# Kernel optimization log

Measured on AMD Instinct MI355X. Metric: run time of the kernel, lower is better.

## Reference

```python
import math
import jax, jax.numpy as jnp
import numpy as np

D, NH, NL, NP = 256, 8, 4, 4
C = D // NH
VALUE_SHAPES = np.array([[128, 128], [64, 64], [32, 32], [16, 16]], dtype=np.int32)


def _offset_bias():
    # Faithful to MSDeformAttn._reset_parameters grid init for sampling_offsets.bias
    th = np.arange(NH, dtype=np.float32) * (2.0 * np.pi / NH)
    g = np.stack([np.cos(th), np.sin(th)], -1)                      # [NH,2]
    g = g / np.abs(g).max(-1, keepdims=True)
    g = np.tile(g[:, None, None, :], (1, NL, NP, 1))                # [NH,NL,NP,2]
    g = g * np.arange(1, NP + 1, dtype=np.float32)[None, None, :, None]
    return jnp.asarray(g.reshape(-1), jnp.float32)


def setup_inputs() -> dict:
    key = jax.random.key(0)
    ks = jax.random.split(key, 10)
    bs, Q = 8, 2048
    LV = int((VALUE_SHAPES[:, 0] * VALUE_SHAPES[:, 1]).sum())
    s = 0.02
    return {
        "query": jax.random.normal(ks[0], (bs, Q, D), jnp.float32),
        "refer_bbox": jax.random.uniform(ks[1], (bs, Q, NL, 2), jnp.float32),
        "value": jax.random.normal(ks[2], (bs, LV, D), jnp.float32),
        "value_shapes": VALUE_SHAPES,  # static numpy (shapes must be compile-time constants)
        "W_value": jax.random.normal(ks[3], (D, D), jnp.float32) * s,
        "b_value": jnp.zeros((D,), jnp.float32),
        "W_off": jax.random.normal(ks[4], (D, NH * NL * NP * 2), jnp.float32) * 0.01,
        "b_off": _offset_bias(),
        "W_attn": jax.random.normal(ks[5], (D, NH * NL * NP), jnp.float32) * s,
        "b_attn": jnp.zeros((NH * NL * NP,), jnp.float32),
        "W_out": jax.random.normal(ks[6], (D, D), jnp.float32) * s,
        "b_out": jnp.zeros((D,), jnp.float32),
    }


def _ms_deform_attn(value, shapes, loc, attn):
    # value: [bs,LV,NH,C], loc: [bs,Q,NH,NL,NP,2] in [0,1], attn: [bs,Q,NH,NL,NP]
    bs, LV = value.shape[:2]
    Q = loc.shape[1]
    BH = bs * NH
    v = value.transpose(0, 2, 1, 3).reshape(BH, LV, C)              # [BH,LV,C]
    loc = loc.transpose(0, 2, 1, 3, 4, 5).reshape(BH, Q, NL, NP, 2)
    attn = attn.transpose(0, 2, 1, 3, 4).reshape(BH, Q, NL, NP)
    acc = jnp.zeros((BH, Q, C), value.dtype)
    start = 0
    for lvl in range(NL):
        H, W = int(shapes[lvl, 0]), int(shapes[lvl, 1])
        img = v[:, start:start + H * W]                             # [BH,HW,C]
        start += H * W
        # grid_sample(align_corners=False): pixel coord = loc * size - 0.5
        x = loc[:, :, lvl, :, 0] * W - 0.5                          # [BH,Q,NP]
        y = loc[:, :, lvl, :, 1] * H - 0.5
        x0 = jnp.floor(x); y0 = jnp.floor(y)
        fx = x - x0; fy = y - y0
        x0i = x0.astype(jnp.int32); y0i = y0.astype(jnp.int32)
        samp = jnp.zeros((BH, Q, NP, C), value.dtype)
        for dx, dy in ((0, 0), (1, 0), (0, 1), (1, 1)):
            xi = x0i + dx; yi = y0i + dy
            valid = (xi >= 0) & (xi < W) & (yi >= 0) & (yi < H)     # zero padding
            w = (fx if dx else 1.0 - fx) * (fy if dy else 1.0 - fy)
            w = jnp.where(valid, w, 0.0)
            idx = jnp.clip(yi, 0, H - 1) * W + jnp.clip(xi, 0, W - 1)
            g = jnp.take_along_axis(img, idx.reshape(BH, Q * NP)[..., None], axis=1)
            samp = samp + w[..., None] * g.reshape(BH, Q, NP, C)
        acc = acc + (samp * attn[:, :, lvl, :, None]).sum(2)
    return acc.reshape(bs, NH, Q, C).transpose(0, 2, 1, 3).reshape(bs, Q, D)


def reference(query, refer_bbox, value, value_shapes, W_value, b_value,
              W_off, b_off, W_attn, b_attn, W_out, b_out):
    shapes = np.asarray(value_shapes)  # static
    bs, Q = query.shape[:2]
    LV = value.shape[1]
    v = (value @ W_value + b_value).reshape(bs, LV, NH, C)
    off = (query @ W_off + b_off).reshape(bs, Q, NH, NL, NP, 2)
    attn = jax.nn.softmax((query @ W_attn + b_attn).reshape(bs, Q, NH, NL * NP), -1)
    attn = attn.reshape(bs, Q, NH, NL, NP)
    norm = jnp.asarray(shapes[:, ::-1], query.dtype)                # (W,H) per level
    loc = refer_bbox[:, :, None, :, None, :] + off / norm[None, None, None, :, None, :]
    out = _ms_deform_attn(v, shapes, loc, attn)
    return out @ W_out + b_out
```

## Files before the change

### kernel.cpp

```cpp
#include <hip/hip_runtime.h>
#include <hip/hip_bf16.h>

#define D_MODEL 256
#define NHEAD   8
#define NLVL    4
#define NPTS    4
#define CH      32
#define QTOT    2048
#define BS      8
#define LVTOT   21760
#define KDIM    256

typedef __attribute__((ext_vector_type(8))) short bf16x8;
typedef __attribute__((ext_vector_type(4))) float f32x4;

__device__ inline float bf_lo(unsigned u) { unsigned t = u << 16; float f; __builtin_memcpy(&f, &t, 4); return f; }
__device__ inline float bf_hi(unsigned u) { unsigned t = u & 0xffff0000u; float f; __builtin_memcpy(&f, &t, 4); return f; }
__device__ inline float bfu2f(unsigned short s) { unsigned t = (unsigned)s << 16; float f; __builtin_memcpy(&f, &t, 4); return f; }
__device__ inline unsigned short f2bfu(float f) { __hip_bfloat16 h = __float2bfloat16(f); unsigned short u; __builtin_memcpy(&u, &h, 2); return u; }

__global__ __launch_bounds__(256)
void convert_W(const float* __restrict__ W, __hip_bfloat16* __restrict__ Wt, int sh) {
    int t = blockIdx.x * 256 + threadIdx.x;
    int k = t >> sh, n = t & ((1 << sh) - 1);
    Wt[n * 256 + k] = __float2bfloat16(W[(k << sh) + n]);
}

__global__ __launch_bounds__(256)
void convert_q(const float* __restrict__ q, __hip_bfloat16* __restrict__ qb) {
    int t = blockIdx.x * 256 + threadIdx.x;
    float4 f = ((const float4*)q)[t];
    __hip_bfloat16 h4[4] = {__float2bfloat16(f.x), __float2bfloat16(f.y),
                            __float2bfloat16(f.z), __float2bfloat16(f.w)};
    ((uint2*)qb)[t] = *(const uint2*)h4;
}

#define BK  64
#define LDP 72
#define LDC2 136

__global__ __launch_bounds__(256, 4)
void gemm_value_mfma(const float* __restrict__ A,
                     const __hip_bfloat16* __restrict__ Wt,
                     const float* __restrict__ bias,
                     __hip_bfloat16* __restrict__ v) {
    __shared__ __align__(16) char smem[128 * LDP * 2 * 2];
    __hip_bfloat16* As = (__hip_bfloat16*)smem;
    __hip_bfloat16* Bs = (__hip_bfloat16*)(smem + 128 * LDP * 2);
    __hip_bfloat16* Cs = (__hip_bfloat16*)smem;

    const int tid  = threadIdx.x;
    const int lane = tid & 63;
    const int wave = tid >> 6;
    const int wr   = wave >> 1;
    const int wc   = wave & 1;
    const int cb      = blockIdx.x * 128;
    const int rowBase = blockIdx.y * 128;

    const int m0   = lane & 15;
    const int quad = lane >> 4;

    const int ar = tid >> 4;
    const int ac = tid & 15;
    const int br = tid >> 3;
    const int bc = tid & 7;

    f32x4 acc[4][4] = {};

    for (int kc = 0; kc < KDIM; kc += BK) {
#pragma unroll
        for (int i = 0; i < 8; ++i) {
            const int row = i * 16 + ar;
            float4 f = *(const float4*)(A + (size_t)(rowBase + row) * KDIM + kc + ac * 4);
            __hip_bfloat16 t4[4] = {__float2bfloat16(f.x), __float2bfloat16(f.y),
                                    __float2bfloat16(f.z), __float2bfloat16(f.w)};
            *(uint2*)&As[row * LDP + ac * 4] = *(const uint2*)t4;
        }
#pragma unroll
        for (int i = 0; i < 4; ++i) {
            const int row = i * 32 + br;
            uint4 u = *(const uint4*)(Wt + (size_t)(cb + row) * KDIM + kc + bc * 8);
            *(uint4*)&Bs[row * LDP + bc * 8] = u;
        }
        __syncthreads();

#pragma unroll
        for (int ks = 0; ks < 2; ++ks) {
            bf16x8 af[4], bfv[4];
#pragma unroll
            for (int i = 0; i < 4; ++i)
                af[i] = *(const bf16x8*)&As[(wr * 64 + i * 16 + m0) * LDP + ks * 32 + quad * 8];
#pragma unroll
            for (int j = 0; j < 4; ++j)
                bfv[j] = *(const bf16x8*)&Bs[(wc * 64 + j * 16 + m0) * LDP + ks * 32 + quad * 8];
#pragma unroll
            for (int i = 0; i < 4; ++i)
#pragma unroll
                for (int j = 0; j < 4; ++j)
                    acc[i][j] = __builtin_amdgcn_mfma_f32_16x16x32_bf16(af[i], bfv[j], acc[i][j], 0, 0, 0);
        }
        __syncthreads();
    }

    const int b = rowBase / LVTOT;
    const int pixBase = rowBase - b * LVTOT;
#pragma unroll
    for (int half = 0; half < 2; ++half) {
        if (wr == half) {
#pragma unroll
            for (int j = 0; j < 4; ++j) {
                const int lcol = wc * 64 + j * 16 + m0;
                const float bv = bias[cb + lcol];
#pragma unroll
                for (int i = 0; i < 4; ++i) {
                    const int lrow = i * 16 + quad * 4;
#pragma unroll
                    for (int r = 0; r < 4; ++r)
                        Cs[(lrow + r) * LDC2 + lcol] = __float2bfloat16(acc[i][j][r] + bv);
                }
            }
        }
        __syncthreads();
        char* dst = (char*)v + (size_t)(b * LVTOT + pixBase + half * 64) * 512 + cb * 2;
        const char* src = (const char*)Cs;
#pragma unroll
        for (int itr = 0; itr < 4; ++itr) {
            const int o = itr * 4096 + tid * 16;
            const int row = o >> 8;
            const int c   = o & 255;
            uint4 val = *(const uint4*)(src + row * (LDC2 * 2) + c);
            *(uint4*)(dst + (size_t)row * 512 + c) = val;
        }
        if (half == 0) __syncthreads();
    }
}

struct StorePlain {
    float* o;
    int ncol;
    __device__ void operator()(int row, int col, float val) const {
        o[(size_t)row * ncol + col] = val;
    }
};

template <typename Store>
__global__ __launch_bounds__(256, 2)
void gemm_bf16_mfma(const __hip_bfloat16* __restrict__ A,
                    const __hip_bfloat16* __restrict__ Wt,
                    const float* __restrict__ bias, Store store) {
    __shared__ __align__(16) __hip_bfloat16 As[128 * LDP];
    __shared__ __align__(16) __hip_bfloat16 Bs[128 * LDP];

    const int tid  = threadIdx.x;
    const int lane = tid & 63;
    const int wave = tid >> 6;
    const int rowBase = blockIdx.x * 128;
    const int cb = blockIdx.y * 128;

    const int m0   = lane & 15;
    const int quad = lane >> 4;

    const int br = tid >> 3;
    const int bc = tid & 7;

    f32x4 acc[2][8] = {};

    for (int kc = 0; kc < KDIM; kc += BK) {
#pragma unroll
        for (int i = 0; i < 4; ++i) {
            const int row = i * 32 + br;
            uint4 ua = *(const uint4*)(A  + (size_t)(rowBase + row) * KDIM + kc + bc * 8);
            uint4 ub = *(const uint4*)(Wt + (size_t)(cb + row) * KDIM + kc + bc * 8);
            *(uint4*)&As[row * LDP + bc * 8] = ua;
            *(uint4*)&Bs[row * LDP + bc * 8] = ub;
        }
        __syncthreads();

#pragma unroll
        for (int ks = 0; ks < 2; ++ks) {
            bf16x8 af[2], bfv[8];
#pragma unroll
            for (int i = 0; i < 2; ++i)
                af[i] = *(const bf16x8*)&As[(wave * 32 + i * 16 + m0) * LDP + ks * 32 + quad * 8];
#pragma unroll
            for (int j = 0; j < 8; ++j)
                bfv[j] = *(const bf16x8*)&Bs[(j * 16 + m0) * LDP + ks * 32 + quad * 8];
#pragma unroll
            for (int i = 0; i < 2; ++i)
#pragma unroll
                for (int j = 0; j < 8; ++j)
                    acc[i][j] = __builtin_amdgcn_mfma_f32_16x16x32_bf16(af[i], bfv[j], acc[i][j], 0, 0, 0);
        }
        __syncthreads();
    }

#pragma unroll
    for (int j = 0; j < 8; ++j) {
        const int col = cb + j * 16 + m0;
        const float bv = bias[col];
#pragma unroll
        for (int i = 0; i < 2; ++i) {
            const int row0 = rowBase + wave * 32 + i * 16 + quad * 4;
#pragma unroll
            for (int r = 0; r < 4; ++r)
                store(row0 + r, col, acc[i][j][r] + bv);
        }
    }
}

__global__ __launch_bounds__(256)
void sample_kernel(const float* __restrict__ off_ws,
                   const float* __restrict__ logits_ws,
                   const float* __restrict__ bbox,
                   const __hip_bfloat16* __restrict__ v,
                   __hip_bfloat16* __restrict__ acc_bf) {
    __shared__ __align__(16) float off_s[8 * 256];
    __shared__ __align__(16) float attn_s[8 * 128];
    __shared__ float bbox_s[64];
    __shared__ __align__(16) int idx_s[1024 * 4];
    __shared__ __align__(8) unsigned short w_s[1024 * 4];

    const int tid = threadIdx.x;
    const int b = blockIdx.x & 7;
    const int gq0 = b * QTOT + (blockIdx.x >> 3) * 8;

    const float4* osrc = (const float4*)(off_ws + (size_t)gq0 * 256);
    ((float4*)off_s)[tid] = osrc[tid];
    ((float4*)off_s)[tid + 256] = osrc[tid + 256];
    const float4* lsrc = (const float4*)(logits_ws + (size_t)gq0 * 128);
    ((float4*)attn_s)[tid] = lsrc[tid];
    if (tid < 64) bbox_s[tid] = bbox[(size_t)gq0 * 8 + tid];
    __syncthreads();

    if (tid < 64) {
        int qq = tid >> 3, h = tid & 7;
        float* p = attn_s + qq * 128 + h * 16;
        float m = p[0];
#pragma unroll
        for (int i = 1; i < 16; ++i) m = fmaxf(m, p[i]);
        float e[16], s = 0.f;
#pragma unroll
        for (int i = 0; i < 16; ++i) { e[i] = __expf(p[i] - m); s += e[i]; }
        float inv = 1.f / s;
#pragma unroll
        for (int i = 0; i < 16; ++i) p[i] = e[i] * inv;
    }
    __syncthreads();

#pragma unroll
    for (int r = 0; r < 4; ++r) {
        const int tap = tid + r * 256;
        const int qq = tap >> 7, h = (tap >> 4) & 7, l = (tap >> 2) & 3, p = tap & 3;
        const int Wd = 128 >> l;
        const int st = (l == 0) ? 0 : (l == 1) ? 16384 : (l == 2) ? 20480 : 21504;

        const float bx = bbox_s[qq * 8 + l * 2 + 0];
        const float by = bbox_s[qq * 8 + l * 2 + 1];
        const float ox = off_s[qq * 256 + h * 32 + l * 8 + p * 2 + 0];
        const float oy = off_s[qq * 256 + h * 32 + l * 8 + p * 2 + 1];
        const float att = attn_s[qq * 128 + h * 16 + l * 4 + p];

        const float x = bx * (float)Wd + ox - 0.5f;
        const float y = by * (float)Wd + oy - 0.5f;
        const float x0f = floorf(x), y0f = floorf(y);
        const float fx = x - x0f, fy = y - y0f;
        const int x0 = (int)x0f, y0 = (int)y0f;
        const int x1 = x0 + 1, y1 = y0 + 1;
        const bool vx0 = (unsigned)x0 < (unsigned)Wd;
        const bool vx1 = (unsigned)x1 < (unsigned)Wd;
        const bool vy0 = (unsigned)y0 < (unsigned)Wd;
        const bool vy1 = (unsigned)y1 < (unsigned)Wd;
        const int cx0 = min(max(x0, 0), Wd - 1), cx1 = min(max(x1, 0), Wd - 1);
        const int cy0 = min(max(y0, 0), Wd - 1), cy1 = min(max(y1, 0), Wd - 1);

        int4 idx;
        idx.x = (st + cy0 * Wd + cx0) << 9;
        idx.y = (st + cy0 * Wd + cx1) << 9;
        idx.z = (st + cy1 * Wd + cx0) << 9;
        idx.w = (st + cy1 * Wd + cx1) << 9;
        float w0 = (vx0 && vy0) ? (1.f - fx) * (1.f - fy) * att : 0.f;
        float w1 = (vx1 && vy0) ? fx * (1.f - fy) * att : 0.f;
        float w2 = (vx0 && vy1) ? (1.f - fx) * fy * att : 0.f;
        float w3 = (vx1 && vy1) ? fx * fy * att : 0.f;

        *(int4*)&idx_s[tap * 4] = idx;
        unsigned short w4[4] = {f2bfu(w0), f2bfu(w1), f2bfu(w2), f2bfu(w3)};
        *(uint2*)&w_s[tap * 4] = *(const uint2*)w4;
    }
    __syncthreads();

    const int lane = tid & 63;
    const int wave = tid >> 6;
    const int g = lane >> 4;
    const int c2 = lane & 15;

    const char* vbase = (const char*)v + (size_t)b * LVTOT * 512 + c2 * 4;

    for (int i = 0; i < 16; ++i) {
        const int pair = wave * 16 + i;
        const int qq = pair >> 3, hh = pair & 7;
        const char* slab = vbase + hh * 64;
        const int tbase = qq * 128 + hh * 16;

        float ax0 = 0.f, ay0 = 0.f, ax1 = 0.f, ay1 = 0.f, ax2 = 0.f, ay2 = 0.f, ax3 = 0.f, ay3 = 0.f;
#pragma unroll
        for (int ts = 0; ts < 4; ++ts) {
            const int tap = tbase + ts * 4 + g;
            const int4 idx = *(const int4*)&idx_s[tap * 4];
            const ushort4 ww = *(const ushort4*)&w_s[tap * 4];
            unsigned u0 = *(const unsigned*)(slab + idx.x);
            unsigned u1 = *(const unsigned*)(slab + idx.y);
            unsigned u2 = *(const unsigned*)(slab + idx.z);
            unsigned u3 = *(const unsigned*)(slab + idx.w);
            float w0 = bfu2f(ww.x), w1 = bfu2f(ww.y), w2 = bfu2f(ww.z), w3 = bfu2f(ww.w);
            ax0 += w0 * bf_lo(u0); ay0 += w0 * bf_hi(u0);
            ax1 += w1 * bf_lo(u1); ay1 += w1 * bf_hi(u1);
            ax2 += w2 * bf_lo(u2); ay2 += w2 * bf_hi(u2);
            ax3 += w3 * bf_lo(u3); ay3 += w3 * bf_hi(u3);
        }
        float sx = (ax0 + ax1) + (ax2 + ax3);
        float sy = (ay0 + ay1) + (ay2 + ay3);
        sx += __shfl_xor(sx, 16); sy += __shfl_xor(sy, 16);
        sx += __shfl_xor(sx, 32); sy += __shfl_xor(sy, 32);
        if (g == 0) {
            __hip_bfloat16 h2[2] = {__float2bfloat16(sx), __float2bfloat16(sy)};
            unsigned packed; __builtin_memcpy(&packed, h2, 4);
            *(unsigned*)((char*)acc_bf + ((size_t)(gq0 + qq) * 256 + hh * 32 + c2 * 2) * 2) = packed;
        }
    }
}

extern "C" void kernel_launch(void* const* d_in, const int* in_sizes, int n_in,
                              void* d_out, int out_size, void* d_ws, size_t ws_size,
                              hipStream_t stream) {
    const float* query   = (const float*)d_in[0];
    const float* bbox    = (const float*)d_in[1];
    const float* value   = (const float*)d_in[2];
    const float* W_value = (const float*)d_in[4];
    const float* b_value = (const float*)d_in[5];
    const float* W_off   = (const float*)d_in[6];
    const float* b_off   = (const float*)d_in[7];
    const float* W_attn  = (const float*)d_in[8];
    const float* b_attn  = (const float*)d_in[9];
    const float* W_out   = (const float*)d_in[10];
    const float* b_out   = (const float*)d_in[11];
    float* out = (float*)d_out;

    char* ws = (char*)d_ws;
    __hip_bfloat16* v_ws  = (__hip_bfloat16*)ws;
    float* off_ws         = (float*)(ws + 89128960);
    float* logits_ws      = (float*)(ws + 89128960 + 16777216);
    __hip_bfloat16* acc_bf = (__hip_bfloat16*)(ws + 89128960 + 16777216 + 8388608);
    __hip_bfloat16* q_bf   = (__hip_bfloat16*)(ws + 89128960 + 16777216 + 8388608 + 8388608);

    __hip_bfloat16* Wt_v    = acc_bf;
    __hip_bfloat16* Wt_off  = acc_bf + 65536;
    __hip_bfloat16* Wt_attn = acc_bf + 131072;
    __hip_bfloat16* Wt_out  = q_bf;

    const int NQ = BS * QTOT;
    const int NVROWS = BS * LVTOT;

    convert_q<<<NQ * KDIM / 1024, 256, 0, stream>>>(query, q_bf);
    convert_W<<<256, 256, 0, stream>>>(W_value, Wt_v, 8);
    convert_W<<<256, 256, 0, stream>>>(W_off, Wt_off, 8);
    convert_W<<<128, 256, 0, stream>>>(W_attn, Wt_attn, 7);

    gemm_value_mfma<<<dim3(2, NVROWS / 128), 256, 0, stream>>>(value, Wt_v, b_value, v_ws);

    gemm_bf16_mfma<<<dim3(NQ / 128, 2), 256, 0, stream>>>(
        q_bf, Wt_off, b_off, StorePlain{off_ws, 256});

    gemm_bf16_mfma<<<dim3(NQ / 128, 1), 256, 0, stream>>>(
        q_bf, Wt_attn, b_attn, StorePlain{logits_ws, 128});

    convert_W<<<256, 256, 0, stream>>>(W_out, Wt_out, 8);

    sample_kernel<<<NQ / 8, 256, 0, stream>>>(off_ws, logits_ws, bbox, v_ws, acc_bf);

    gemm_bf16_mfma<<<dim3(NQ / 128, 2), 256, 0, stream>>>(
        acc_bf, Wt_out, b_out, StorePlain{out, 256});
}
```

Baseline: 415.8 us.

## Merge offset/attention GEMMs and retile value and query GEMMs

The value-projection GEMM now loads a K-chunk of 128 per iteration, so there are two chunks and fewer barriers. This doubles its LDS use and lowers the occupancy hint from 4 to 2. The offset and attention-logit GEMMs are merged into one launch over the concatenated transposed weights (Wt_attn sits contiguously after Wt_off), with a split store that routes columns to two buffers. The query-side GEMMs use a smaller 64x128 tile with a 2x2 wave layout to raise block count and occupancy, and the bias add moves into the store functors.

```diff
diff --git a/kernel.cpp b/kernel.cpp
--- a/kernel.cpp
+++ b/kernel.cpp
@@ -35,18 +35,17 @@
     ((uint2*)qb)[t] = *(const uint2*)h4;
 }
 
-#define BK  64
+#define LDV 136
 #define LDP 72
-#define LDC2 136
-
-__global__ __launch_bounds__(256, 4)
+
+__global__ __launch_bounds__(256, 2)
 void gemm_value_mfma(const float* __restrict__ A,
                      const __hip_bfloat16* __restrict__ Wt,
                      const float* __restrict__ bias,
                      __hip_bfloat16* __restrict__ v) {
-    __shared__ __align__(16) char smem[128 * LDP * 2 * 2];
+    __shared__ __align__(16) char smem[2 * 128 * LDV * 2];
     __hip_bfloat16* As = (__hip_bfloat16*)smem;
-    __hip_bfloat16* Bs = (__hip_bfloat16*)(smem + 128 * LDP * 2);
+    __hip_bfloat16* Bs = (__hip_bfloat16*)(smem + 128 * LDV * 2);
     __hip_bfloat16* Cs = (__hip_bfloat16*)smem;
 
     const int tid  = threadIdx.x;
@@ -60,39 +59,34 @@
     const int m0   = lane & 15;
     const int quad = lane >> 4;
 
-    const int ar = tid >> 4;
-    const int ac = tid & 15;
-    const int br = tid >> 3;
-    const int bc = tid & 7;
-
     f32x4 acc[4][4] = {};
 
-    for (int kc = 0; kc < KDIM; kc += BK) {
-#pragma unroll
-        for (int i = 0; i < 8; ++i) {
-            const int row = i * 16 + ar;
-            float4 f = *(const float4*)(A + (size_t)(rowBase + row) * KDIM + kc + ac * 4);
+    for (int kc = 0; kc < KDIM; kc += 128) {
+#pragma unroll
+        for (int it = 0; it < 16; ++it) {
+            const int row = it * 8 + (tid >> 5);
+            float4 f = *(const float4*)(A + (size_t)(rowBase + row) * KDIM + kc + (tid & 31) * 4);
             __hip_bfloat16 t4[4] = {__float2bfloat16(f.x), __float2bfloat16(f.y),
                                     __float2bfloat16(f.z), __float2bfloat16(f.w)};
-            *(uint2*)&As[row * LDP + ac * 4] = *(const uint2*)t4;
-        }
-#pragma unroll
-        for (int i = 0; i < 4; ++i) {
-            const int row = i * 32 + br;
-            uint4 u = *(const uint4*)(Wt + (size_t)(cb + row) * KDIM + kc + bc * 8);
-            *(uint4*)&Bs[row * LDP + bc * 8] = u;
-        }
-        __syncthreads();
-
-#pragma unroll
-        for (int ks = 0; ks < 2; ++ks) {
+            *(uint2*)&As[row * LDV + (tid & 31) * 4] = *(const uint2*)t4;
+        }
+#pragma unroll
+        for (int it = 0; it < 8; ++it) {
+            const int row = it * 16 + (tid >> 4);
+            uint4 u = *(const uint4*)(Wt + (size_t)(cb + row) * KDIM + kc + (tid & 15) * 8);
+            *(uint4*)&Bs[row * LDV + (tid & 15) * 8] = u;
+        }
+        __syncthreads();
+
+#pragma unroll
+        for (int ks = 0; ks < 4; ++ks) {
             bf16x8 af[4], bfv[4];
 #pragma unroll
             for (int i = 0; i < 4; ++i)
-                af[i] = *(const bf16x8*)&As[(wr * 64 + i * 16 + m0) * LDP + ks * 32 + quad * 8];
+                af[i] = *(const bf16x8*)&As[(wr * 64 + i * 16 + m0) * LDV + ks * 32 + quad * 8];
 #pragma unroll
             for (int j = 0; j < 4; ++j)
-                bfv[j] = *(const bf16x8*)&Bs[(wc * 64 + j * 16 + m0) * LDP + ks * 32 + quad * 8];
+                bfv[j] = *(const bf16x8*)&Bs[(wc * 64 + j * 16 + m0) * LDV + ks * 32 + quad * 8];
 #pragma unroll
             for (int i = 0; i < 4; ++i)
 #pragma unroll
@@ -116,7 +110,7 @@
                     const int lrow = i * 16 + quad * 4;
 #pragma unroll
                     for (int r = 0; r < 4; ++r)
-                        Cs[(lrow + r) * LDC2 + lcol] = __float2bfloat16(acc[i][j][r] + bv);
+                        Cs[(lrow + r) * LDV + lcol] = __float2bfloat16(acc[i][j][r] + bv);
                 }
             }
         }
@@ -128,7 +122,7 @@
             const int o = itr * 4096 + tid * 16;
             const int row = o >> 8;
             const int c   = o & 255;
-            uint4 val = *(const uint4*)(src + row * (LDC2 * 2) + c);
+            uint4 val = *(const uint4*)(src + row * (LDV * 2) + c);
             *(uint4*)(dst + (size_t)row * 512 + c) = val;
         }
         if (half == 0) __syncthreads();
@@ -138,72 +132,88 @@
 struct StorePlain {
     float* o;
     int ncol;
+    const float* bias;
     __device__ void operator()(int row, int col, float val) const {
-        o[(size_t)row * ncol + col] = val;
+        o[(size_t)row * ncol + col] = val + bias[col];
     }
 };
 
+struct StoreSplit {
+    float* o1;
+    float* o2;
+    const float* b1;
+    const float* b2;
+    __device__ void operator()(int row, int col, float val) const {
+        if (col < 256) o1[(size_t)row * 256 + col] = val + b1[col];
+        else           o2[(size_t)row * 128 + (col - 256)] = val + b2[col - 256];
+    }
+};
+
 template <typename Store>
-__global__ __launch_bounds__(256, 2)
-void gemm_bf16_mfma(const __hip_bfloat16* __restrict__ A,
-                    const __hip_bfloat16* __restrict__ Wt,
-                    const float* __restrict__ bias, Store store) {
-    __shared__ __align__(16) __hip_bfloat16 As[128 * LDP];
+__global__ __launch_bounds__(256, 4)
+void gemm_bf16_small(const __hip_bfloat16* __restrict__ A,
+                     const __hip_bfloat16* __restrict__ Wt, Store store) {
+    __shared__ __align__(16) __hip_bfloat16 As[64 * LDP];
     __shared__ __align__(16) __hip_bfloat16 Bs[128 * LDP];
 
     const int tid  = threadIdx.x;
     const int lane = tid & 63;
     const int wave = tid >> 6;
-    const int rowBase = blockIdx.x * 128;
-    const int cb = blockIdx.y * 128;
+    const int wr   = wave >> 1;
+    const int wc   = wave & 1;
+    const int rowBase = blockIdx.x * 64;
+    const int cb      = blockIdx.y * 128;
 
     const int m0   = lane & 15;
     const int quad = lane >> 4;
 
-    const int br = tid >> 3;
-    const int bc = tid & 7;
-
-    f32x4 acc[2][8] = {};
-
-    for (int kc = 0; kc < KDIM; kc += BK) {
-#pragma unroll
-        for (int i = 0; i < 4; ++i) {
-            const int row = i * 32 + br;
-            uint4 ua = *(const uint4*)(A  + (size_t)(rowBase + row) * KDIM + kc + bc * 8);
-            uint4 ub = *(const uint4*)(Wt + (size_t)(cb + row) * KDIM + kc + bc * 8);
-            *(uint4*)&As[row * LDP + bc * 8] = ua;
-            *(uint4*)&Bs[row * LDP + bc * 8] = ub;
+    const int sr = tid >> 3;
+    const int sc = tid & 7;
+
+    f32x4 acc[2][4] = {};
+
+    for (int kc = 0; kc < KDIM; kc += 64) {
+#pragma unroll
+        for (int it = 0; it < 2; ++it) {
+            const int row = it * 32 + sr;
+            uint4 ua = *(const uint4*)(A + (size_t)(rowBase + row) * KDIM + kc + sc * 8);
+            *(uint4*)&As[row * LDP + sc * 8] = ua;
+        }
+#pragma unroll
+        for (int it = 0; it < 4; ++it) {
+            const int row = it * 32 + sr;
+            uint4 ub = *(const uint4*)(Wt + (size_t)(cb + row) * KDIM + kc + sc * 8);
+            *(uint4*)&Bs[row * LDP + sc * 8] = ub;
         }
         __syncthreads();
 
 #pragma unroll
         for (int ks = 0; ks < 2; ++ks) {
-            bf16x8 af[2], bfv[8];
+            bf16x8 af[2], bfv[4];
 #pragma unroll
             for (int i = 0; i < 2; ++i)
-                af[i] = *(const bf16x8*)&As[(wave * 32 + i * 16 + m0) * LDP + ks * 32 + quad * 8];
-#pragma unroll
-            for (int j = 0; j < 8; ++j)
-                bfv[j] = *(const bf16x8*)&Bs[(j * 16 + m0) * LDP + ks * 32 + quad * 8];
+                af[i] = *(const bf16x8*)&As[(wr * 32 + i * 16 + m0) * LDP + ks * 32 + quad * 8];
+#pragma unroll
+            for (int j = 0; j < 4; ++j)
+                bfv[j] = *(const bf16x8*)&Bs[(wc * 64 + j * 16 + m0) * LDP + ks * 32 + quad * 8];
 #pragma unroll
             for (int i = 0; i < 2; ++i)
 #pragma unroll
-                for (int j = 0; j < 8; ++j)
+                for (int j = 0; j < 4; ++j)
                     acc[i][j] = __builtin_amdgcn_mfma_f32_16x16x32_bf16(af[i], bfv[j], acc[i][j], 0, 0, 0);
         }
         __syncthreads();
     }
 
 #pragma unroll
-    for (int j = 0; j < 8; ++j) {
-        const int col = cb + j * 16 + m0;
-        const float bv = bias[col];
+    for (int j = 0; j < 4; ++j) {
+        const int col = cb + wc * 64 + j * 16 + m0;
 #pragma unroll
         for (int i = 0; i < 2; ++i) {
-            const int row0 = rowBase + wave * 32 + i * 16 + quad * 4;
+            const int row0 = rowBase + wr * 32 + i * 16 + quad * 4;
 #pragma unroll
             for (int r = 0; r < 4; ++r)
-                store(row0 + r, col, acc[i][j][r] + bv);
+                store(row0 + r, col, acc[i][j][r]);
         }
     }
 }
@@ -368,16 +378,13 @@
 
     gemm_value_mfma<<<dim3(2, NVROWS / 128), 256, 0, stream>>>(value, Wt_v, b_value, v_ws);
 
-    gemm_bf16_mfma<<<dim3(NQ / 128, 2), 256, 0, stream>>>(
-        q_bf, Wt_off, b_off, StorePlain{off_ws, 256});
-
-    gemm_bf16_mfma<<<dim3(NQ / 128, 1), 256, 0, stream>>>(
-        q_bf, Wt_attn, b_attn, StorePlain{logits_ws, 128});
+    gemm_bf16_small<<<dim3(NQ / 64, 3), 256, 0, stream>>>(
+        q_bf, Wt_off, StoreSplit{off_ws, logits_ws, b_off, b_attn});
 
     convert_W<<<256, 256, 0, stream>>>(W_out, Wt_out, 8);
 
     sample_kernel<<<NQ / 8, 256, 0, stream>>>(off_ws, logits_ws, bbox, v_ws, acc_bf);
 
-    gemm_bf16_mfma<<<dim3(NQ / 128, 2), 256, 0, stream>>>(
-        acc_bf, Wt_out, b_out, StorePlain{out, 256});
-}
+    gemm_bf16_small<<<dim3(NQ / 64, 2), 256, 0, stream>>>(
+        acc_bf, Wt_out, StorePlain{out, 256, b_out});
+}
```

After: 411.3 us. Within noise of the previous version (-1.1%).

## Merge conversion kernels and fuse value/offset/attention GEMMs into one launch

Applied to the files above, without the earlier changes.

Replaces the four separate conversion launches with one block-partitioned convert_all kernel. The value projection and the offset and attention-logit GEMMs now run as a single fused_gemms launch that dispatches on block index. The offset and attention GEMMs are merged into one 384-column GEMM, relying on Wt_off and Wt_attn sitting contiguously in memory. This cuts launch overhead and lets the small GEMMs overlap with the large value GEMM. The value body now runs under launch_bounds(256,2) instead of (256,4), which may lower its occupancy.

```diff
diff --git a/kernel.cpp b/kernel.cpp
--- a/kernel.cpp
+++ b/kernel.cpp
@@ -19,6 +19,40 @@
 __device__ inline float bfu2f(unsigned short s) { unsigned t = (unsigned)s << 16; float f; __builtin_memcpy(&f, &t, 4); return f; }
 __device__ inline unsigned short f2bfu(float f) { __hip_bfloat16 h = __float2bfloat16(f); unsigned short u; __builtin_memcpy(&u, &h, 2); return u; }
 
+#define BK  64
+#define LDP 72
+#define LDC2 136
+
+__device__ inline void transpose_W_body(const float* __restrict__ W,
+                                        __hip_bfloat16* __restrict__ Wt,
+                                        int sh, int blk, int tid) {
+    int t = blk * 256 + tid;
+    int k = t >> sh, n = t & ((1 << sh) - 1);
+    Wt[n * 256 + k] = __float2bfloat16(W[(k << sh) + n]);
+}
+
+__global__ __launch_bounds__(256)
+void convert_all(const float* __restrict__ q, __hip_bfloat16* __restrict__ qb,
+                 const float* __restrict__ Wv, __hip_bfloat16* __restrict__ Wtv,
+                 const float* __restrict__ Wo, __hip_bfloat16* __restrict__ Wto,
+                 const float* __restrict__ Wa, __hip_bfloat16* __restrict__ Wta) {
+    const int bid = blockIdx.x;
+    const int tid = threadIdx.x;
+    if (bid < 4096) {
+        int t = bid * 256 + tid;
+        float4 f = ((const float4*)q)[t];
+        __hip_bfloat16 h4[4] = {__float2bfloat16(f.x), __float2bfloat16(f.y),
+                                __float2bfloat16(f.z), __float2bfloat16(f.w)};
+        ((uint2*)qb)[t] = *(const uint2*)h4;
+    } else if (bid < 4352) {
+        transpose_W_body(Wv, Wtv, 8, bid - 4096, tid);
+    } else if (bid < 4608) {
+        transpose_W_body(Wo, Wto, 8, bid - 4352, tid);
+    } else {
+        transpose_W_body(Wa, Wta, 7, bid - 4608, tid);
+    }
+}
+
 __global__ __launch_bounds__(256)
 void convert_W(const float* __restrict__ W, __hip_bfloat16* __restrict__ Wt, int sh) {
     int t = blockIdx.x * 256 + threadIdx.x;
@@ -26,25 +60,11 @@
     Wt[n * 256 + k] = __float2bfloat16(W[(k << sh) + n]);
 }
 
-__global__ __launch_bounds__(256)
-void convert_q(const float* __restrict__ q, __hip_bfloat16* __restrict__ qb) {
-    int t = blockIdx.x * 256 + threadIdx.x;
-    float4 f = ((const float4*)q)[t];
-    __hip_bfloat16 h4[4] = {__float2bfloat16(f.x), __float2bfloat16(f.y),
-                            __float2bfloat16(f.z), __float2bfloat16(f.w)};
-    ((uint2*)qb)[t] = *(const uint2*)h4;
-}
-
-#define BK  64
-#define LDP 72
-#define LDC2 136
-
-__global__ __launch_bounds__(256, 4)
-void gemm_value_mfma(const float* __restrict__ A,
-                     const __hip_bfloat16* __restrict__ Wt,
-                     const float* __restrict__ bias,
-                     __hip_bfloat16* __restrict__ v) {
-    __shared__ __align__(16) char smem[128 * LDP * 2 * 2];
+__device__ void value_gemm_body(char* smem, int bid_v,
+                                const float* __restrict__ A,
+                                const __hip_bfloat16* __restrict__ Wt,
+                                const float* __restrict__ bias,
+                                __hip_bfloat16* __restrict__ v) {
     __hip_bfloat16* As = (__hip_bfloat16*)smem;
     __hip_bfloat16* Bs = (__hip_bfloat16*)(smem + 128 * LDP * 2);
     __hip_bfloat16* Cs = (__hip_bfloat16*)smem;
@@ -54,8 +74,8 @@
     const int wave = tid >> 6;
     const int wr   = wave >> 1;
     const int wc   = wave & 1;
-    const int cb      = blockIdx.x * 128;
-    const int rowBase = blockIdx.y * 128;
+    const int cb      = (bid_v & 1) * 128;
+    const int rowBase = (bid_v >> 1) * 128;
 
     const int m0   = lane & 15;
     const int quad = lane >> 4;
@@ -132,6 +152,97 @@
             *(uint4*)(dst + (size_t)row * 512 + c) = val;
         }
         if (half == 0) __syncthreads();
+    }
+}
+
+__device__ void offattn_gemm_body(char* smem, int bid,
+                                  const __hip_bfloat16* __restrict__ A,
+                                  const __hip_bfloat16* __restrict__ Wt_oa,
+                                  const float* __restrict__ b_off,
+                                  const float* __restrict__ b_attn,
+                                  float* __restrict__ off_ws,
+                                  float* __restrict__ logits_ws) {
+    __hip_bfloat16* As = (__hip_bfloat16*)smem;
+    __hip_bfloat16* Bs = (__hip_bfloat16*)(smem + 128 * LDP * 2);
+
+    const int tid  = threadIdx.x;
+    const int lane = tid & 63;
+    const int wave = tid >> 6;
+    const int rowBase = (bid & 127) * 128;
+    const int cb      = (bid >> 7) * 128;
+
+    const int m0   = lane & 15;
+    const int quad = lane >> 4;
+
+    const int br = tid >> 3;
+    const int bc = tid & 7;
+
+    f32x4 acc[2][8] = {};
+
+    for (int kc = 0; kc < KDIM; kc += BK) {
+#pragma unroll
+        for (int i = 0; i < 4; ++i) {
+            const int row = i * 32 + br;
+            uint4 ua = *(const uint4*)(A     + (size_t)(rowBase + row) * KDIM + kc + bc * 8);
+            uint4 ub = *(const uint4*)(Wt_oa + (size_t)(cb + row) * KDIM + kc + bc * 8);
+            *(uint4*)&As[row * LDP + bc * 8] = ua;
+            *(uint4*)&Bs[row * LDP + bc * 8] = ub;
+        }
+        __syncthreads();
+
+#pragma unroll
+        for (int ks = 0; ks < 2; ++ks) {
+            bf16x8 af[2], bfv[8];
+#pragma unroll
+            for (int i = 0; i < 2; ++i)
+                af[i] = *(const bf16x8*)&As[(wave * 32 + i * 16 + m0) * LDP + ks * 32 + quad * 8];
+#pragma unroll
+            for (int j = 0; j < 8; ++j)
+                bfv[j] = *(const bf16x8*)&Bs[(j * 16 + m0) * LDP + ks * 32 + quad * 8];
+#pragma unroll
+            for (int i = 0; i < 2; ++i)
+#pragma unroll
+                for (int j = 0; j < 8; ++j)
+                    acc[i][j] = __builtin_amdgcn_mfma_f32_16x16x32_bf16(af[i], bfv[j], acc[i][j], 0, 0, 0);
+        }
+        __syncthreads();
+    }
+
+#pragma unroll
+    for (int j = 0; j < 8; ++j) {
+        const int col = cb + j * 16 + m0;
+        const bool isOff = (col < 256);
+        const float bv = isOff ? b_off[col] : b_attn[col - 256];
+#pragma unroll
+        for (int i = 0; i < 2; ++i) {
+            const int row0 = rowBase + wave * 32 + i * 16 + quad * 4;
+#pragma unroll
+            for (int r = 0; r < 4; ++r) {
+                const float val = acc[i][j][r] + bv;
+                if (isOff) off_ws[(size_t)(row0 + r) * 256 + col] = val;
+                else       logits_ws[(size_t)(row0 + r) * 128 + (col - 256)] = val;
+            }
+        }
+    }
+}
+
+__global__ __launch_bounds__(256, 2)
+void fused_gemms(const float* __restrict__ value,
+                 const __hip_bfloat16* __restrict__ Wt_v,
+                 const float* __restrict__ b_value,
+                 __hip_bfloat16* __restrict__ v_ws,
+                 const __hip_bfloat16* __restrict__ q_bf,
+                 const __hip_bfloat16* __restrict__ Wt_oa,
+                 const float* __restrict__ b_off,
+                 const float* __restrict__ b_attn,
+                 float* __restrict__ off_ws,
+                 float* __restrict__ logits_ws) {
+    __shared__ __align__(16) char smem[36864];
+    const int bid = blockIdx.x;
+    if (bid < 384) {
+        offattn_gemm_body(smem, bid, q_bf, Wt_oa, b_off, b_attn, off_ws, logits_ws);
+    } else {
+        value_gemm_body(smem, bid - 384, value, Wt_v, b_value, v_ws);
     }
 }
 
@@ -361,18 +472,14 @@
     const int NQ = BS * QTOT;
     const int NVROWS = BS * LVTOT;
 
-    convert_q<<<NQ * KDIM / 1024, 256, 0, stream>>>(query, q_bf);
-    convert_W<<<256, 256, 0, stream>>>(W_value, Wt_v, 8);
-    convert_W<<<256, 256, 0, stream>>>(W_off, Wt_off, 8);
-    convert_W<<<128, 256, 0, stream>>>(W_attn, Wt_attn, 7);
-
-    gemm_value_mfma<<<dim3(2, NVROWS / 128), 256, 0, stream>>>(value, Wt_v, b_value, v_ws);
-
-    gemm_bf16_mfma<<<dim3(NQ / 128, 2), 256, 0, stream>>>(
-        q_bf, Wt_off, b_off, StorePlain{off_ws, 256});
-
-    gemm_bf16_mfma<<<dim3(NQ / 128, 1), 256, 0, stream>>>(
-        q_bf, Wt_attn, b_attn, StorePlain{logits_ws, 128});
+    convert_all<<<4736, 256, 0, stream>>>(query, q_bf,
+                                          W_value, Wt_v,
+                                          W_off, Wt_off,
+                                          W_attn, Wt_attn);
+
+    fused_gemms<<<384 + 2 * (NVROWS / 128), 256, 0, stream>>>(
+        value, Wt_v, b_value, v_ws,
+        q_bf, Wt_off, b_off, b_attn, off_ws, logits_ws);
 
     convert_W<<<256, 256, 0, stream>>>(W_out, Wt_out, 8);
 
```

Result: faster. 390.5 us (-6.1%).
